# Kernel optimization log

Measured on AMD Instinct MI355X. Metric: run time of the kernel, lower is better.

## Reference

```python
import jax, jax.numpy as jnp
import numpy as np

MV = 16          # multivector dimension (PGA G(3,0,1))
BLADE_LEN = 9    # number of equivariant basis maps
# inner-product mask: coordinates not containing e0 (scalar, e1,e2,e3, e12,e13,e23, e123)
IP_IDX = np.array([0, 2, 3, 4, 8, 9, 10, 14])


def equi_linear(w, blade, x):
    """EquiLinearLayer: einsum('j i b, b x y, ... i x -> ... j y').
    Precompute blade-contracted weight once (fusion the kernel would do)."""
    wb = jnp.einsum('jib,bxy->jixy', w, blade)          # [J, I, MV, MV]
    return jnp.einsum('jixy,...ix->...jy', wb, x)        # [..., J, MV]


def setup_inputs() -> dict:
    key = jax.random.key(0)
    ks = jax.random.split(key, 6)
    B, N, C = 2, 2048, 64       # batch, items, mv_channels
    D, H = 64, 8                # hidden_dim, n_heads
    x = jax.random.normal(ks[0], (B, N, C, MV), dtype=jnp.float32)
    blade = jax.random.normal(ks[1], (BLADE_LEN, MV, MV), dtype=jnp.float32)
    w_q = jax.random.uniform(ks[2], (D * H, C, BLADE_LEN), dtype=jnp.float32)
    w_k = jax.random.uniform(ks[3], (D, C, BLADE_LEN), dtype=jnp.float32)
    w_v = jax.random.uniform(ks[4], (D, C, BLADE_LEN), dtype=jnp.float32)
    w_o = jax.random.uniform(ks[5], (C, D * H, BLADE_LEN), dtype=jnp.float32)
    return {"x": x, "blade": blade, "w_q": w_q, "w_k": w_k, "w_v": w_v, "w_o": w_o}


def reference(x, blade, w_q, w_k, w_v, w_o):
    B, N, C, _ = x.shape
    D = w_k.shape[0]
    H = w_q.shape[0] // D

    q = equi_linear(w_q, blade, x)   # [B, N, D*H, MV]
    k = equi_linear(w_k, blade, x)   # [B, N, D, MV]
    v = equi_linear(w_v, blade, x)   # [B, N, D, MV]

    # '(hidden_dim n_heads)' split: hidden_dim outer, heads inner
    q = q.reshape(B, N, D, H, MV).transpose(0, 3, 1, 2, 4)   # [B, H, N, D, MV]

    # select inner-product coordinates and flatten channel x coord
    qm = q[..., IP_IDX].reshape(B, H, N, D * len(IP_IDX))    # [B, H, N, D*8]
    km = k[..., IP_IDX].reshape(B, N, D * len(IP_IDX))        # [B, N, D*8]
    vf = v.reshape(B, N, D * MV)                              # [B, N, D*16]

    scale = 1.0 / jnp.sqrt(jnp.asarray(qm.shape[-1], qm.dtype))
    scores = jnp.einsum('bhqe,bke->bhqk', qm, km) * scale     # [B, H, N, N]
    attn = jax.nn.softmax(scores, axis=-1)
    out = jnp.einsum('bhqk,bkf->bhqf', attn, vf)              # [B, H, N, D*16]

    # slice first hidden_dim*mv (a no-op here since v keeps all 16 coords)
    out = out[..., : D * MV].reshape(B, H, N, D, MV)
    # '(heads hidden_dim)': heads outer
    out = out.transpose(0, 2, 1, 3, 4).reshape(B, N, H * D, MV)

    return equi_linear(w_o, blade, out)                       # [B, N, out_channels, MV]
```

## Files before the change

kernel.cpp:

```cpp
#include <hip/hip_runtime.h>
#include <math.h>


typedef __bf16 bf16x8 __attribute__((ext_vector_type(8)));
typedef __bf16 bf16x4 __attribute__((ext_vector_type(4)));
typedef float floatx4 __attribute__((ext_vector_type(4)));
typedef float floatx16 __attribute__((ext_vector_type(16)));

__constant__ int c_ip[8] = {0, 2, 3, 4, 8, 9, 10, 14};

__global__ __launch_bounds__(256) void prep2(
    const float* __restrict__ x, const float* __restrict__ blade,
    const float* __restrict__ w_q, const float* __restrict__ w_k,
    const float* __restrict__ w_v, const float* __restrict__ w_o,
    __bf16* __restrict__ xh, __bf16* __restrict__ xl,
    __bf16* __restrict__ wbqkh, __bf16* __restrict__ wbqkl,
    __bf16* __restrict__ wbv, __bf16* __restrict__ wbo)
{
  __shared__ float sw[4608];
  __shared__ float sbl[144];
  const int blk = blockIdx.x;
  const int tid = threadIdx.x;

  if (blk < 4608) {
    int n = blk;
    const float* wrow;
    int y;
    if (n < 4096) {
      int e = n & 7, d = (n >> 3) & 63, h = n >> 9;
      wrow = w_q + (size_t)(d * 8 + h) * 576;
      y = c_ip[e];
    } else {
      int n2 = n - 4096;
      int e = n2 & 7, d = n2 >> 3;
      wrow = w_k + (size_t)d * 576;
      y = c_ip[e];
    }
    for (int t = tid; t < 576; t += 256) sw[t] = wrow[t];
    if (tid < 144) sbl[tid] = blade[(tid >> 4) * 256 + (tid & 15) * 16 + y];
    __syncthreads();
#pragma unroll
    for (int kq = 0; kq < 4; kq++) {
      int k = kq * 256 + tid;
      int i = k >> 4, xx = k & 15;
      float s = 0.f;
#pragma unroll
      for (int b = 0; b < 9; b++) s += sw[i * 9 + b] * sbl[b * 16 + xx];
      __bf16 h16 = (__bf16)s;
      wbqkh[(size_t)n * 1024 + k] = h16;
      wbqkl[(size_t)n * 1024 + k] = (__bf16)(s - (float)h16);
    }
  } else if (blk < 5632) {
    int n = blk - 4608;
    int d = n >> 4, y = n & 15;
    const float* wrow = w_v + (size_t)d * 576;
    for (int t = tid; t < 576; t += 256) sw[t] = wrow[t];
    if (tid < 144) sbl[tid] = blade[(tid >> 4) * 256 + (tid & 15) * 16 + y];
    __syncthreads();
#pragma unroll
    for (int kq = 0; kq < 4; kq++) {
      int k = kq * 256 + tid;
      int i = k >> 4, xx = k & 15;
      float s = 0.f;
#pragma unroll
      for (int b = 0; b < 9; b++) s += sw[i * 9 + b] * sbl[b * 16 + xx];
      wbv[(size_t)n * 1024 + k] = (__bf16)s;
    }
  } else if (blk < 6656) {
    int n = blk - 5632;
    int c = n >> 4, y = n & 15;
    const float* wrow = w_o + (size_t)c * 4608;
    for (int t = tid; t < 4608; t += 256) sw[t] = wrow[t];
    if (tid < 144) sbl[tid] = blade[(tid >> 4) * 256 + (tid & 15) * 16 + y];
    __syncthreads();
#pragma unroll
    for (int kq = 0; kq < 32; kq++) {
      int k = kq * 256 + tid;
      int ich = (k >> 10) * 64 + ((k >> 4) & 63);
      int mv = k & 15;
      float s = 0.f;
#pragma unroll
      for (int b = 0; b < 9; b++) s += sw[ich * 9 + b] * sbl[b * 16 + mv];
      wbo[(size_t)n * 8192 + k] = (__bf16)s;
    }
  } else {
    int idx = (blk - 6656) * 256 + tid;
    float4 v = ((const float4*)x)[idx];
    bf16x4 h, l;
    h.x = (__bf16)v.x; l.x = (__bf16)(v.x - (float)h.x);
    h.y = (__bf16)v.y; l.y = (__bf16)(v.y - (float)h.y);
    h.z = (__bf16)v.z; l.z = (__bf16)(v.z - (float)h.z);
    h.w = (__bf16)v.w; l.w = (__bf16)(v.w - (float)h.w);
    *(bf16x4*)(xh + (size_t)idx * 4) = h;
    *(bf16x4*)(xl + (size_t)idx * 4) = l;
  }
}

__global__ __launch_bounds__(256) void reduce4(
    const float* __restrict__ p, float* __restrict__ out, int n)
{
  int i = (blockIdx.x * 256 + threadIdx.x) * 4;
  if (i >= n) return;
  float4 a = *(const float4*)(p + i);
  float4 b = *(const float4*)(p + (size_t)n + i);
  float4 c = *(const float4*)(p + 2 * (size_t)n + i);
  float4 d = *(const float4*)(p + 3 * (size_t)n + i);
  *(float4*)(out + i) = make_float4(a.x + b.x + c.x + d.x, a.y + b.y + c.y + d.y,
                                    a.z + b.z + c.z + d.z, a.w + b.w + c.w + d.w);
}

static __device__ __forceinline__ void gll16(const __bf16* g, __bf16* l) {
  __builtin_amdgcn_global_load_lds(
      (const __attribute__((address_space(1))) void*)g,
      (__attribute__((address_space(3))) void*)l, 16, 0, 0);
}

template <int GROUP, int TS>
static __device__ __forceinline__ void swizzle_mn(int& m0, int& n0) {
  int gn = gridDim.x;
  int flat = blockIdx.y * gn + blockIdx.x;
  int panel = flat / (GROUP * gn);
  int r = flat - panel * GROUP * gn;
  m0 = (panel * GROUP + (r % GROUP)) * TS;
  n0 = (r / GROUP) * TS;
}

template <int GROUP, int TSM, int TSN>
static __device__ __forceinline__ void swizzle_mn2(int& m0, int& n0) {
  int gn = gridDim.x;
  int flat = blockIdx.y * gn + blockIdx.x;
  int panel = flat / (GROUP * gn);
  int r = flat - panel * GROUP * gn;
  m0 = (panel * GROUP + (r % GROUP)) * TSM;
  n0 = (r / GROUP) * TSN;
}

static __device__ __forceinline__ int frag_off32(int row, int t, int kh) {
  return row * 32 + 8 * ((2 * t + kh) ^ ((row >> 1) & 3));
}

template <int EPI>
__global__ __launch_bounds__(256) void gemm_bf16(
    const __bf16* __restrict__ A, int lda, long long sAz,
    const __bf16* __restrict__ Bt, int ldb, long long sBz,
    void* __restrict__ C0v, int ldc, long long sCz,
    int K, float alpha)
{
  __shared__ __bf16 As[128 * 32];
  __shared__ __bf16 Bs[128 * 32];
  const int tid = threadIdx.x;
  const int wave = tid >> 6, lane = tid & 63;
  int m0, n0;
  swizzle_mn<4, 128>(m0, n0);
  A  += (size_t)blockIdx.z * sAz;
  Bt += (size_t)blockIdx.z * sBz;

  const int srow = lane >> 2;
  const int skk = 8 * ((lane & 3) ^ ((lane >> 3) & 3));
  const __bf16* gA0 = A  + (size_t)(m0 + wave * 32      + srow) * lda + skk;
  const __bf16* gA1 = A  + (size_t)(m0 + wave * 32 + 16 + srow) * lda + skk;
  const __bf16* gB0 = Bt + (size_t)(n0 + wave * 32      + srow) * ldb + skk;
  const __bf16* gB1 = Bt + (size_t)(n0 + wave * 32 + 16 + srow) * ldb + skk;
  const int ldsoff = wave * 1024;

  const int l31 = lane & 31, kh = lane >> 5;
  const int wm = (wave & 1) * 64, wn = (wave >> 1) * 64;
  int aoff[2][2], boff[2][2];
#pragma unroll
  for (int i = 0; i < 2; i++)
#pragma unroll
    for (int t = 0; t < 2; t++) {
      aoff[i][t] = frag_off32(wm + i * 32 + l31, t, kh);
      boff[i][t] = frag_off32(wn + i * 32 + l31, t, kh);
    }

  floatx16 acc[2][2];
#pragma unroll
  for (int i = 0; i < 2; i++)
#pragma unroll
    for (int j = 0; j < 2; j++)
#pragma unroll
      for (int e = 0; e < 16; e++) acc[i][j][e] = 0.f;

  for (int k0 = 0; k0 < K; k0 += 32) {
    gll16(gA0, As + ldsoff); gll16(gA1, As + ldsoff + 512);
    gll16(gB0, Bs + ldsoff); gll16(gB1, Bs + ldsoff + 512);
    gA0 += 32; gA1 += 32; gB0 += 32; gB1 += 32;
    __syncthreads();
    bf16x8 af[2][2], bfv[2][2];
#pragma unroll
    for (int i = 0; i < 2; i++)
#pragma unroll
      for (int t = 0; t < 2; t++) {
        af[i][t]  = *(const bf16x8*)(As + aoff[i][t]);
        bfv[i][t] = *(const bf16x8*)(Bs + boff[i][t]);
      }
#pragma unroll
    for (int t = 0; t < 2; t++)
#pragma unroll
      for (int i = 0; i < 2; i++)
#pragma unroll
        for (int j = 0; j < 2; j++)
          acc[i][j] = __builtin_amdgcn_mfma_f32_32x32x16_bf16(
              af[i][t], bfv[j][t], acc[i][j], 0, 0, 0);
    __syncthreads();
  }

  const int rb = m0 + wm + 4 * kh;
  const int cb = n0 + wn + l31;
#pragma unroll
  for (int i = 0; i < 2; i++) {
#pragma unroll
    for (int j = 0; j < 2; j++) {
      int c = cb + j * 32;
#pragma unroll
      for (int q = 0; q < 4; q++) {
        int r = rb + i * 32 + 8 * q;
        float v0 = acc[i][j][q * 4 + 0] * alpha;
        float v1 = acc[i][j][q * 4 + 1] * alpha;
        float v2 = acc[i][j][q * 4 + 2] * alpha;
        float v3 = acc[i][j][q * 4 + 3] * alpha;
        if (EPI == 0) {
          float* C = (float*)C0v + (size_t)blockIdx.z * sCz;
          float* p = C + (size_t)r * ldc + c;
          p[0] = v0; p[ldc] = v1; p[2 * ldc] = v2; p[3 * ldc] = v3;
        } else {
          __bf16* C = (__bf16*)C0v + (size_t)blockIdx.z * sCz;
          C[(size_t)r * ldc + c] = (__bf16)v0;
          C[(size_t)(r + 1) * ldc + c] = (__bf16)v1;
          C[(size_t)(r + 2) * ldc + c] = (__bf16)v2;
          C[(size_t)(r + 3) * ldc + c] = (__bf16)v3;
        }
      }
    }
  }
}

template <int EPI>
__global__ __launch_bounds__(256) void gemm_split(
    const __bf16* __restrict__ Ah, const __bf16* __restrict__ Al, int lda, long long sAz,
    const __bf16* __restrict__ Bh, const __bf16* __restrict__ Bl, int ldb, long long sBz,
    void* __restrict__ C0v, void* __restrict__ C1v, int ldc, long long sCz,
    int K, float alpha)
{
  __shared__ __bf16 Ash[128 * 32];
  __shared__ __bf16 Asl[128 * 32];
  __shared__ __bf16 Bsh[128 * 32];
  __shared__ __bf16 Bsl[128 * 32];
  const int tid = threadIdx.x;
  const int wave = tid >> 6, lane = tid & 63;
  int m0, n0;
  swizzle_mn<8, 128>(m0, n0);
  Ah += (size_t)blockIdx.z * sAz;
  Al += (size_t)blockIdx.z * sAz;
  Bh += (size_t)blockIdx.z * sBz;
  Bl += (size_t)blockIdx.z * sBz;

  const int srow = lane >> 2;
  const int skk = 8 * ((lane & 3) ^ ((lane >> 3) & 3));
  const size_t ao0 = (size_t)(m0 + wave * 32      + srow) * lda + skk;
  const size_t ao1 = (size_t)(m0 + wave * 32 + 16 + srow) * lda + skk;
  const size_t bo0 = (size_t)(n0 + wave * 32      + srow) * ldb + skk;
  const size_t bo1 = (size_t)(n0 + wave * 32 + 16 + srow) * ldb + skk;
  const __bf16 *gAh0 = Ah + ao0, *gAh1 = Ah + ao1;
  const __bf16 *gAl0 = Al + ao0, *gAl1 = Al + ao1;
  const __bf16 *gBh0 = Bh + bo0, *gBh1 = Bh + bo1;
  const __bf16 *gBl0 = Bl + bo0, *gBl1 = Bl + bo1;
  const int ldsoff = wave * 1024;

  const int fr = lane & 15, fq = lane >> 4;
  const int wm = (wave & 1) * 64, wn = (wave >> 1) * 64;
  int aoff[4], boff[4];
#pragma unroll
  for (int t = 0; t < 4; t++) {
    int rA = wm + t * 16 + fr;
    aoff[t] = rA * 32 + 8 * (fq ^ ((rA >> 1) & 3));
    int rB = wn + t * 16 + fr;
    boff[t] = rB * 32 + 8 * (fq ^ ((rB >> 1) & 3));
  }

  floatx4 acc[4][4];
#pragma unroll
  for (int i = 0; i < 4; i++)
#pragma unroll
    for (int j = 0; j < 4; j++) acc[i][j] = (floatx4){0.f, 0.f, 0.f, 0.f};

  for (int k0 = 0; k0 < K; k0 += 32) {
    gll16(gAh0, Ash + ldsoff); gll16(gAh1, Ash + ldsoff + 512);
    gll16(gAl0, Asl + ldsoff); gll16(gAl1, Asl + ldsoff + 512);
    gll16(gBh0, Bsh + ldsoff); gll16(gBh1, Bsh + ldsoff + 512);
    gll16(gBl0, Bsl + ldsoff); gll16(gBl1, Bsl + ldsoff + 512);
    gAh0 += 32; gAh1 += 32; gAl0 += 32; gAl1 += 32;
    gBh0 += 32; gBh1 += 32; gBl0 += 32; gBl1 += 32;
    __syncthreads();
    bf16x8 afh[4], afl[4], bfh[4], bfl[4];
#pragma unroll
    for (int t = 0; t < 4; t++) {
      afh[t] = *(const bf16x8*)(Ash + aoff[t]);
      afl[t] = *(const bf16x8*)(Asl + aoff[t]);
      bfh[t] = *(const bf16x8*)(Bsh + boff[t]);
      bfl[t] = *(const bf16x8*)(Bsl + boff[t]);
    }
#pragma unroll
    for (int i = 0; i < 4; i++)
#pragma unroll
      for (int j = 0; j < 4; j++) {
        acc[i][j] = __builtin_amdgcn_mfma_f32_16x16x32_bf16(
            afh[i], bfh[j], acc[i][j], 0, 0, 0);
        acc[i][j] = __builtin_amdgcn_mfma_f32_16x16x32_bf16(
            afl[i], bfh[j], acc[i][j], 0, 0, 0);
        acc[i][j] = __builtin_amdgcn_mfma_f32_16x16x32_bf16(
            afh[i], bfl[j], acc[i][j], 0, 0, 0);
      }
    __syncthreads();
  }

  const int rb = m0 + wm + fq * 4;
  const int cb = n0 + wn + fr;
#pragma unroll
  for (int i = 0; i < 4; i++) {
#pragma unroll
    for (int j = 0; j < 4; j++) {
      float vv[4] = {acc[i][j].x * alpha, acc[i][j].y * alpha,
                     acc[i][j].z * alpha, acc[i][j].w * alpha};
      int r = rb + i * 16, c = cb + j * 16;
      if (EPI == 0) {
        float* C = (float*)C0v + (size_t)blockIdx.z * sCz;
        float* p = C + (size_t)r * ldc + c;
        p[0] = vv[0]; p[ldc] = vv[1]; p[2 * ldc] = vv[2]; p[3 * ldc] = vv[3];
      } else {
        __bf16* Hp = (__bf16*)C0v + (size_t)blockIdx.z * sCz;
        __bf16* Lp = (__bf16*)C1v + (size_t)blockIdx.z * sCz;
#pragma unroll
        for (int t = 0; t < 4; t++) {
          size_t o = (size_t)(r + t) * ldc + c;
          __bf16 hh = (__bf16)vv[t];
          Hp[o] = hh;
          Lp[o] = (__bf16)(vv[t] - (float)hh);
        }
      }
    }
  }
}

#define MFMA1(a, b, c) c = __builtin_amdgcn_mfma_f32_16x16x32_bf16(a, b, c, 0, 0, 0)

#define MFMA_PAIR2(A0H, A0L, A1H, A1L, i0, i1)                              \
  __builtin_amdgcn_s_setprio(1);                                            \
  _Pragma("unroll") for (int j = 0; j < 4; j++) {                           \
    MFMA1(A0H, bh[j], acc[i0][j]); MFMA1(A1H, bh[j], acc[i1][j]);           \
    MFMA1(A0L, bh[j], acc[i0][j]); MFMA1(A1L, bh[j], acc[i1][j]);           \
    MFMA1(A0H, bl[j], acc[i0][j]); MFMA1(A1H, bl[j], acc[i1][j]);           \
  }                                                                         \
  __builtin_amdgcn_s_setprio(0)

#define TILE8P(SAh, SAl, SBh, SBl, DAh, DAl, DBh, DBl, PF)                  \
  do {                                                                      \
    bf16x8 bh[4], bl[4];                                                    \
    _Pragma("unroll") for (int j = 0; j < 4; j++) {                         \
      bh[j] = *(const bf16x8*)(SBh + boff[j]);                              \
      bl[j] = *(const bf16x8*)(SBl + boff[j]);                              \
    }                                                                       \
    bf16x8 a0h0 = *(const bf16x8*)(SAh + aoff[0]);                          \
    bf16x8 a0l0 = *(const bf16x8*)(SAl + aoff[0]);                          \
    bf16x8 a1h0 = *(const bf16x8*)(SAh + aoff[1]);                          \
    bf16x8 a1l0 = *(const bf16x8*)(SAl + aoff[1]);                          \
                  \
    bf16x8 a0h1 = *(const bf16x8*)(SAh + aoff[2]);                          \
    bf16x8 a0l1 = *(const bf16x8*)(SAl + aoff[2]);                          \
    bf16x8 a1h1 = *(const bf16x8*)(SAh + aoff[3]);                          \
    bf16x8 a1l1 = *(const bf16x8*)(SAl + aoff[3]);                          \
    if (PF) { gll16(pAh0, DAh + lw); gll16(pAh1, DAh + lw + 512);           \
              gll16(pAl0, DAl + lw);                                        \
              pAh0 += 32; pAh1 += 32; pAl0 += 32; }                         \
    MFMA_PAIR2(a0h0, a0l0, a1h0, a1l0, 0, 1);                               \
                  \
    bf16x8 a0h2 = *(const bf16x8*)(SAh + aoff[4]);                          \
    bf16x8 a0l2 = *(const bf16x8*)(SAl + aoff[4]);                          \
    bf16x8 a1h2 = *(const bf16x8*)(SAh + aoff[5]);                          \
    bf16x8 a1l2 = *(const bf16x8*)(SAl + aoff[5]);                          \
    if (PF) { gll16(pAl1, DAl + lw + 512);                                  \
              gll16(pBh0, DBh + lw); gll16(pBh1, DBh + lw + 512);           \
              pAl1 += 32; pBh0 += 32; pBh1 += 32; }                         \
    MFMA_PAIR2(a0h1, a0l1, a1h1, a1l1, 2, 3);                               \
                  \
    bf16x8 a0h3 = *(const bf16x8*)(SAh + aoff[6]);                          \
    bf16x8 a0l3 = *(const bf16x8*)(SAl + aoff[6]);                          \
    bf16x8 a1h3 = *(const bf16x8*)(SAh + aoff[7]);                          \
    bf16x8 a1l3 = *(const bf16x8*)(SAl + aoff[7]);                          \
    if (PF) { gll16(pBl0, DBl + lw); gll16(pBl1, DBl + lw + 512);           \
              pBl0 += 32; pBl1 += 32; }                                     \
    MFMA_PAIR2(a0h2, a0l2, a1h2, a1l2, 4, 5);                               \
                          \
    MFMA_PAIR2(a0h3, a0l3, a1h3, a1l3, 6, 7);                               \
    __syncthreads();                                                        \
  } while (0)

template <int EPI>
__global__ __launch_bounds__(512) void gemm_split_8p(
    const __bf16* __restrict__ Ah, const __bf16* __restrict__ Al, int lda, long long sAz,
    const __bf16* __restrict__ Bh, const __bf16* __restrict__ Bl, int ldb, long long sBz,
    void* __restrict__ C0v, void* __restrict__ C1v, int ldc, long long sCz,
    int K, float alpha)
{
  __shared__ __bf16 sAh0[256 * 32], sAl0[256 * 32], sBh0[256 * 32], sBl0[256 * 32];
  __shared__ __bf16 sAh1[256 * 32], sAl1[256 * 32], sBh1[256 * 32], sBl1[256 * 32];
  const int tid = threadIdx.x;
  const int wave = tid >> 6, lane = tid & 63;
  int m0, n0;
  swizzle_mn<4, 256>(m0, n0);
  Ah += (size_t)blockIdx.z * sAz;
  Al += (size_t)blockIdx.z * sAz;
  Bh += (size_t)blockIdx.z * sBz;
  Bl += (size_t)blockIdx.z * sBz;

  const int srow = lane >> 2;
  const int skk = 8 * ((lane & 3) ^ ((lane >> 3) & 3));
  const __bf16* pAh0 = Ah + (size_t)(m0 + wave * 32 + srow) * lda + skk;
  const __bf16* pAh1 = pAh0 + (size_t)16 * lda;
  const __bf16* pAl0 = Al + (size_t)(m0 + wave * 32 + srow) * lda + skk;
  const __bf16* pAl1 = pAl0 + (size_t)16 * lda;
  const __bf16* pBh0 = Bh + (size_t)(n0 + wave * 32 + srow) * ldb + skk;
  const __bf16* pBh1 = pBh0 + (size_t)16 * ldb;
  const __bf16* pBl0 = Bl + (size_t)(n0 + wave * 32 + srow) * ldb + skk;
  const __bf16* pBl1 = pBl0 + (size_t)16 * ldb;
  const int lw = wave * 1024;

  const int fr = lane & 15, fq = lane >> 4;
  const int wm = (wave >> 2) * 128, wn = (wave & 3) * 64;
  int aoff[8], boff[4];
#pragma unroll
  for (int i = 0; i < 8; i++) {
    int rA = wm + i * 16 + fr;
    aoff[i] = rA * 32 + 8 * (fq ^ ((rA >> 1) & 3));
  }
#pragma unroll
  for (int j = 0; j < 4; j++) {
    int rB = wn + j * 16 + fr;
    boff[j] = rB * 32 + 8 * (fq ^ ((rB >> 1) & 3));
  }

  floatx4 acc[8][4];
#pragma unroll
  for (int i = 0; i < 8; i++)
#pragma unroll
    for (int j = 0; j < 4; j++) acc[i][j] = (floatx4){0.f, 0.f, 0.f, 0.f};

  const int ktiles = K >> 5;

  gll16(pAh0, sAh0 + lw); gll16(pAh1, sAh0 + lw + 512); pAh0 += 32; pAh1 += 32;
  gll16(pAl0, sAl0 + lw); gll16(pAl1, sAl0 + lw + 512); pAl0 += 32; pAl1 += 32;
  gll16(pBh0, sBh0 + lw); gll16(pBh1, sBh0 + lw + 512); pBh0 += 32; pBh1 += 32;
  gll16(pBl0, sBl0 + lw); gll16(pBl1, sBl0 + lw + 512); pBl0 += 32; pBl1 += 32;
  __syncthreads();

  for (int it = 0; it < (ktiles >> 1); ++it) {
    TILE8P(sAh0, sAl0, sBh0, sBl0, sAh1, sAl1, sBh1, sBl1,
           (2 * it + 1 < ktiles));
    TILE8P(sAh1, sAl1, sBh1, sBl1, sAh0, sAl0, sBh0, sBl0,
           (2 * it + 2 < ktiles));
  }

  const int rb = m0 + wm + fq * 4;
  const int cb = n0 + wn + fr;
#pragma unroll
  for (int i = 0; i < 8; i++) {
#pragma unroll
    for (int j = 0; j < 4; j++) {
      int r = rb + i * 16, c = cb + j * 16;
      float vv[4] = {acc[i][j].x * alpha, acc[i][j].y * alpha,
                     acc[i][j].z * alpha, acc[i][j].w * alpha};
      if (EPI == 0) {
        float* C = (float*)C0v + (size_t)blockIdx.z * sCz;
        float* p = C + (size_t)r * ldc + c;
        p[0] = vv[0]; p[ldc] = vv[1]; p[2 * ldc] = vv[2]; p[3 * ldc] = vv[3];
      } else {
        __bf16* Hp = (__bf16*)C0v + (size_t)blockIdx.z * sCz;
        __bf16* Lp = (__bf16*)C1v + (size_t)blockIdx.z * sCz;
#pragma unroll
        for (int t = 0; t < 4; t++) {
          size_t o = (size_t)(r + t) * ldc + c;
          __bf16 hh = (__bf16)vv[t];
          Hp[o] = hh;
          Lp[o] = (__bf16)(vv[t] - (float)hh);
        }
      }
    }
  }
}

#define PTILE(SA0, SA1, SB0, SB1, DA0, DA1, DB0, DB1, PF)                   \
  do {                                                                      \
    bf16x8 b0[4], b1[4];                                                    \
    _Pragma("unroll") for (int j = 0; j < 4; j++)                           \
      b0[j] = *(const bf16x8*)(SB0 + boff[j]);                              \
    bf16x8 a00 = *(const bf16x8*)(SA0 + aoff[0]);                           \
    bf16x8 a10 = *(const bf16x8*)(SA0 + aoff[1]);                           \
       \
    _Pragma("unroll") for (int j = 0; j < 4; j++)                           \
      b1[j] = *(const bf16x8*)(SB1 + boff[j]);                              \
    bf16x8 a01 = *(const bf16x8*)(SA1 + aoff[0]);                           \
    bf16x8 a11 = *(const bf16x8*)(SA1 + aoff[1]);                           \
    if (PF) { gll16(pA0, DA0 + lw); gll16(pA1, DA0 + lw + 512); }           \
    __builtin_amdgcn_s_setprio(1);                                          \
    _Pragma("unroll") for (int j = 0; j < 4; j++) {                         \
      MFMA1(a00, b0[j], acc[0][j]); MFMA1(a10, b0[j], acc[1][j]);           \
    }                                                                       \
    __builtin_amdgcn_s_setprio(0);                                          \
            \
    bf16x8 a20 = *(const bf16x8*)(SA0 + aoff[2]);                           \
    bf16x8 a30 = *(const bf16x8*)(SA0 + aoff[3]);                           \
    if (PF) { gll16(pA0 + 32, DA1 + lw); gll16(pA1 + 32, DA1 + lw + 512);   \
              pA0 += 64; pA1 += 64; }                                       \
    __builtin_amdgcn_s_setprio(1);                                          \
    _Pragma("unroll") for (int j = 0; j < 4; j++) {                         \
      MFMA1(a01, b1[j], acc[0][j]); MFMA1(a11, b1[j], acc[1][j]);           \
    }                                                                       \
    __builtin_amdgcn_s_setprio(0);                                          \
            \
    bf16x8 a21 = *(const bf16x8*)(SA1 + aoff[2]);                           \
    bf16x8 a31 = *(const bf16x8*)(SA1 + aoff[3]);                           \
    if (PF) { gll16(pB0, DB0 + lwB); gll16(pB0 + 32, DB1 + lwB);            \
              pB0 += 64; }                                                  \
    __builtin_amdgcn_s_setprio(1);                                          \
    _Pragma("unroll") for (int j = 0; j < 4; j++) {                         \
      MFMA1(a20, b0[j], acc[2][j]); MFMA1(a30, b0[j], acc[3][j]);           \
    }                                                                       \
    __builtin_amdgcn_s_setprio(0);                                          \
                  \
    __builtin_amdgcn_s_setprio(1);                                          \
    _Pragma("unroll") for (int j = 0; j < 4; j++) {                         \
      MFMA1(a21, b1[j], acc[2][j]); MFMA1(a31, b1[j], acc[3][j]);           \
    }                                                                       \
    __builtin_amdgcn_s_setprio(0);                                          \
    __syncthreads();                                                        \
  } while (0)

template <int EPI>
__global__ __launch_bounds__(512) void gemm_bf16_8p(
    const __bf16* __restrict__ A, int lda, long long sAz,
    const __bf16* __restrict__ Bt, int ldb, long long sBz,
    void* __restrict__ C0v, int ldc, long long sCz,
    int K, float alpha)
{
  __shared__ __bf16 sA0_0[256 * 32], sA1_0[256 * 32];
  __shared__ __bf16 sB0_0[128 * 32], sB1_0[128 * 32];
  __shared__ __bf16 sA0_1[256 * 32], sA1_1[256 * 32];
  __shared__ __bf16 sB0_1[128 * 32], sB1_1[128 * 32];
  const int tid = threadIdx.x;
  const int wave = tid >> 6, lane = tid & 63;
  int m0, n0;
  swizzle_mn2<4, 256, 128>(m0, n0);
  A  += (size_t)blockIdx.z * sAz;
  Bt += (size_t)blockIdx.z * sBz;

  const int srow = lane >> 2;
  const int skk = 8 * ((lane & 3) ^ ((lane >> 3) & 3));
  const __bf16* pA0 = A + (size_t)(m0 + wave * 32 + srow) * lda + skk;
  const __bf16* pA1 = pA0 + (size_t)16 * lda;
  const __bf16* pB0 = Bt + (size_t)(n0 + wave * 16 + srow) * ldb + skk;
  const int lw = wave * 1024;
  const int lwB = wave * 512;

  const int fr = lane & 15, fq = lane >> 4;
  const int wm = (wave >> 1) * 64, wn = (wave & 1) * 64;
  int aoff[4], boff[4];
#pragma unroll
  for (int i = 0; i < 4; i++) {
    int rA = wm + i * 16 + fr;
    aoff[i] = rA * 32 + 8 * (fq ^ ((rA >> 1) & 3));
    int rB = wn + i * 16 + fr;
    boff[i] = rB * 32 + 8 * (fq ^ ((rB >> 1) & 3));
  }

  floatx4 acc[4][4];
#pragma unroll
  for (int i = 0; i < 4; i++)
#pragma unroll
    for (int j = 0; j < 4; j++) acc[i][j] = (floatx4){0.f, 0.f, 0.f, 0.f};

  const int ktiles = K >> 6;

  gll16(pA0, sA0_0 + lw); gll16(pA1, sA0_0 + lw + 512);
  gll16(pA0 + 32, sA1_0 + lw); gll16(pA1 + 32, sA1_0 + lw + 512);
  gll16(pB0, sB0_0 + lwB); gll16(pB0 + 32, sB1_0 + lwB);
  pA0 += 64; pA1 += 64; pB0 += 64;
  __syncthreads();

  for (int it = 0; it < (ktiles >> 1); ++it) {
    PTILE(sA0_0, sA1_0, sB0_0, sB1_0, sA0_1, sA1_1, sB0_1, sB1_1,
          (2 * it + 1 < ktiles));
    PTILE(sA0_1, sA1_1, sB0_1, sB1_1, sA0_0, sA1_0, sB0_0, sB1_0,
          (2 * it + 2 < ktiles));
  }

  const int rb = m0 + wm + fq * 4;
  const int cb = n0 + wn + fr;
#pragma unroll
  for (int i = 0; i < 4; i++) {
#pragma unroll
    for (int j = 0; j < 4; j++) {
      int r = rb + i * 16, c = cb + j * 16;
      float vv[4] = {acc[i][j].x * alpha, acc[i][j].y * alpha,
                     acc[i][j].z * alpha, acc[i][j].w * alpha};
      if (EPI == 0) {
        float* C = (float*)C0v + (size_t)blockIdx.z * sCz;
        float* p = C + (size_t)r * ldc + c;
        p[0] = vv[0]; p[ldc] = vv[1]; p[2 * ldc] = vv[2]; p[3 * ldc] = vv[3];
      } else {
        __bf16* C = (__bf16*)C0v + (size_t)blockIdx.z * sCz;
        C[(size_t)r * ldc + c] = (__bf16)vv[0];
        C[(size_t)(r + 1) * ldc + c] = (__bf16)vv[1];
        C[(size_t)(r + 2) * ldc + c] = (__bf16)vv[2];
        C[(size_t)(r + 3) * ldc + c] = (__bf16)vv[3];
      }
    }
  }
}

__global__ __launch_bounds__(256) void softmax_wave(float* __restrict__ Pf)
{
  const int wave = threadIdx.x >> 6, lane = threadIdx.x & 63;
  const size_t row = (size_t)blockIdx.x * 4 + wave;
  float* p = Pf + row * 2048;
  __bf16* q = (__bf16*)p;

  float4 v[8];
  float m = -1e30f;
#pragma unroll
  for (int t = 0; t < 8; t++) {
    v[t] = ((const float4*)p)[lane + t * 64];
    m = fmaxf(m, fmaxf(fmaxf(v[t].x, v[t].y), fmaxf(v[t].z, v[t].w)));
  }
#pragma unroll
  for (int off = 32; off; off >>= 1) m = fmaxf(m, __shfl_xor(m, off, 64));

  float s = 0.f;
#pragma unroll
  for (int t = 0; t < 8; t++) {
    v[t].x = expf(v[t].x - m); v[t].y = expf(v[t].y - m);
    v[t].z = expf(v[t].z - m); v[t].w = expf(v[t].w - m);
    s += (v[t].x + v[t].y) + (v[t].z + v[t].w);
  }
#pragma unroll
  for (int off = 32; off; off >>= 1) s += __shfl_xor(s, off, 64);
  float inv = 1.0f / s;

#pragma unroll
  for (int t = 0; t < 8; t++) {
    bf16x4 o;
    o.x = (__bf16)(v[t].x * inv); o.y = (__bf16)(v[t].y * inv);
    o.z = (__bf16)(v[t].z * inv); o.w = (__bf16)(v[t].w * inv);
    *(bf16x4*)(q + (lane + t * 64) * 4) = o;
  }
}

extern "C" void kernel_launch(void* const* d_in, const int* in_sizes, int n_in,
                              void* d_out, int out_size, void* d_ws, size_t ws_size,
                              hipStream_t stream)
{
  (void)in_sizes; (void)n_in; (void)out_size; (void)ws_size;
  const float* x     = (const float*)d_in[0];
  const float* blade = (const float*)d_in[1];
  const float* w_q   = (const float*)d_in[2];
  const float* w_k   = (const float*)d_in[3];
  const float* w_v   = (const float*)d_in[4];
  const float* w_o   = (const float*)d_in[5];
  float* out = (float*)d_out;

  char* base = (char*)d_ws;
  __bf16* wbo   = (__bf16*)(base);
  __bf16* vT    = (__bf16*)(base + 16777216);
  __bf16* qkmh  = (__bf16*)(base + 25165824);
  __bf16* qkml  = (__bf16*)(base + 62914560);
  char* scr = base + 100663296;
  __bf16* xh    = (__bf16*)(scr);
  __bf16* xl    = (__bf16*)(scr + 8388608);
  __bf16* wbqkh = (__bf16*)(scr + 16777216);
  __bf16* wbqkl = (__bf16*)(scr + 26214400);
  __bf16* wbv   = (__bf16*)(scr + 35651584);
  float*  Pf    = (float*)(scr);
  __bf16* A2    = (__bf16*)(scr + 67108864);
  float*  Part  = (float*)(scr + 100663296);

  dim3 blk(256);
  const float scale = 0.04419417382415922f;

  prep2<<<10752, blk, 0, stream>>>(x, blade, w_q, w_k, w_v, w_o,
                                   xh, xl, wbqkh, wbqkl, wbv, wbo);

  gemm_split_8p<2><<<dim3(16, 16, 1), dim3(512), 0, stream>>>(
      xh, xl, 1024, 0, wbqkh, wbqkl, 1024, 0,
      qkmh, qkml, 4608, 0, 1024, 1.f);

  gemm_split<2><<<dim3(4, 32, 1), blk, 0, stream>>>(
      xh, xl, 1024, 0,
      wbqkh + (size_t)4096 * 1024, wbqkl + (size_t)4096 * 1024, 1024, 0,
      qkmh + 4096, qkml + 4096, 4608, 0, 1024, 1.f);

  gemm_bf16<3><<<dim3(32, 8, 1), blk, 0, stream>>>(
      wbv, 1024, 0, xh, 1024, 0, vT, 4096, 0, 1024, 1.f);

  for (int b = 0; b < 2; b++) {
    const __bf16* qh_b  = qkmh + (size_t)b * 2048 * 4608;
    const __bf16* ql_b  = qkml + (size_t)b * 2048 * 4608;
    const __bf16* kmh_b = qh_b + 4096;
    const __bf16* kml_b = ql_b + 4096;

    for (int h0 = 0; h0 < 8; h0 += 4) {
      gemm_split_8p<0><<<dim3(8, 8, 4), dim3(512), 0, stream>>>(
          qh_b + h0 * 512, ql_b + h0 * 512, 4608, 512,
          kmh_b, kml_b, 4608, 0,
          Pf, nullptr, 2048, (long long)2048 * 2048, 512, scale);
      softmax_wave<<<4 * 2048 / 4, blk, 0, stream>>>(Pf);
      gemm_bf16_8p<3><<<dim3(8, 8, 4), dim3(512), 0, stream>>>(
          (const __bf16*)Pf, 4096, (long long)2048 * 4096,
          vT + (size_t)b * 2048, 4096, 0,
          A2 + (size_t)h0 * 1024, 8192, 1024, 2048, 1.f);
    }

    gemm_bf16_8p<0><<<dim3(8, 8, 4), dim3(512), 0, stream>>>(
        A2, 8192, 2048, wbo, 8192, 2048,
        Part, 1024, (long long)2048 * 1024, 2048, 1.f);
    reduce4<<<2048, blk, 0, stream>>>(Part, out + (size_t)b * 2048 * 1024,
                                      2048 * 1024);
  }
}
```

Baseline: 737.0 us.

## Switch split-bf16 GEMM to 32x32x16 MFMA tiles and reorder PTILE fragment loads

```diff
diff --git a/kernel.cpp b/kernel.cpp
--- a/kernel.cpp
+++ b/kernel.cpp
@@ -343,56 +343,64 @@
   }
 }
 
-#define MFMA1(a, b, c) c = __builtin_amdgcn_mfma_f32_16x16x32_bf16(a, b, c, 0, 0, 0)
-
-#define MFMA_PAIR2(A0H, A0L, A1H, A1L, i0, i1)                              \
+#define MFMA32(a, b, c) c = __builtin_amdgcn_mfma_f32_32x32x16_bf16(a, b, c, 0, 0, 0)
+
+#define MFMA_FRAG32(I)                                                      \
   __builtin_amdgcn_s_setprio(1);                                            \
-  _Pragma("unroll") for (int j = 0; j < 4; j++) {                           \
-    MFMA1(A0H, bh[j], acc[i0][j]); MFMA1(A1H, bh[j], acc[i1][j]);           \
-    MFMA1(A0L, bh[j], acc[i0][j]); MFMA1(A1L, bh[j], acc[i1][j]);           \
-    MFMA1(A0H, bl[j], acc[i0][j]); MFMA1(A1H, bl[j], acc[i1][j]);           \
-  }                                                                         \
+  MFMA32(ah0, bh00, acc[I][0]); MFMA32(ah0, bh10, acc[I][1]);               \
+  MFMA32(al0, bh00, acc[I][0]); MFMA32(al0, bh10, acc[I][1]);               \
+  MFMA32(ah0, bl00, acc[I][0]); MFMA32(ah0, bl10, acc[I][1]);               \
+  MFMA32(ah1, bh01, acc[I][0]); MFMA32(ah1, bh11, acc[I][1]);               \
+  MFMA32(al1, bh01, acc[I][0]); MFMA32(al1, bh11, acc[I][1]);               \
+  MFMA32(ah1, bl01, acc[I][0]); MFMA32(ah1, bl11, acc[I][1]);               \
   __builtin_amdgcn_s_setprio(0)
 
 #define TILE8P(SAh, SAl, SBh, SBl, DAh, DAl, DBh, DBl, PF)                  \
   do {                                                                      \
-    bf16x8 bh[4], bl[4];                                                    \
-    _Pragma("unroll") for (int j = 0; j < 4; j++) {                         \
-      bh[j] = *(const bf16x8*)(SBh + boff[j]);                              \
-      bl[j] = *(const bf16x8*)(SBl + boff[j]);                              \
+    bf16x8 bh00 = *(const bf16x8*)(SBh + boff[0][0]);                       \
+    bf16x8 bh01 = *(const bf16x8*)(SBh + boff[0][1]);                       \
+    bf16x8 bh10 = *(const bf16x8*)(SBh + boff[1][0]);                       \
+    bf16x8 bh11 = *(const bf16x8*)(SBh + boff[1][1]);                       \
+    bf16x8 bl00 = *(const bf16x8*)(SBl + boff[0][0]);                       \
+    bf16x8 bl01 = *(const bf16x8*)(SBl + boff[0][1]);                       \
+    bf16x8 bl10 = *(const bf16x8*)(SBl + boff[1][0]);                       \
+    bf16x8 bl11 = *(const bf16x8*)(SBl + boff[1][1]);                       \
+    {                              \
+      bf16x8 ah0 = *(const bf16x8*)(SAh + aoff[0][0]);                      \
+      bf16x8 ah1 = *(const bf16x8*)(SAh + aoff[0][1]);                      \
+      bf16x8 al0 = *(const bf16x8*)(SAl + aoff[0][0]);                      \
+      bf16x8 al1 = *(const bf16x8*)(SAl + aoff[0][1]);                      \
+      if (PF) { gll16(pAh0, DAh + lw); gll16(pAh1, DAh + lw + 512);         \
+                gll16(pAl0, DAl + lw);                                      \
+                pAh0 += 32; pAh1 += 32; pAl0 += 32; }                       \
+      MFMA_FRAG32(0);                                                       \
     }                                                                       \
-    bf16x8 a0h0 = *(const bf16x8*)(SAh + aoff[0]);                          \
-    bf16x8 a0l0 = *(const bf16x8*)(SAl + aoff[0]);                          \
-    bf16x8 a1h0 = *(const bf16x8*)(SAh + aoff[1]);                          \
-    bf16x8 a1l0 = *(const bf16x8*)(SAl + aoff[1]);                          \
-                  \
-    bf16x8 a0h1 = *(const bf16x8*)(SAh + aoff[2]);                          \
-    bf16x8 a0l1 = *(const bf16x8*)(SAl + aoff[2]);                          \
-    bf16x8 a1h1 = *(const bf16x8*)(SAh + aoff[3]);                          \
-    bf16x8 a1l1 = *(const bf16x8*)(SAl + aoff[3]);                          \
-    if (PF) { gll16(pAh0, DAh + lw); gll16(pAh1, DAh + lw + 512);           \
-              gll16(pAl0, DAl + lw);                                        \
-              pAh0 += 32; pAh1 += 32; pAl0 += 32; }                         \
-    MFMA_PAIR2(a0h0, a0l0, a1h0, a1l0, 0, 1);                               \
-                  \
-    bf16x8 a0h2 = *(const bf16x8*)(SAh + aoff[4]);                          \
-    bf16x8 a0l2 = *(const bf16x8*)(SAl + aoff[4]);                          \
-    bf16x8 a1h2 = *(const bf16x8*)(SAh + aoff[5]);                          \
-    bf16x8 a1l2 = *(const bf16x8*)(SAl + aoff[5]);                          \
-    if (PF) { gll16(pAl1, DAl + lw + 512);                                  \
-              gll16(pBh0, DBh + lw); gll16(pBh1, DBh + lw + 512);           \
-              pAl1 += 32; pBh0 += 32; pBh1 += 32; }                         \
-    MFMA_PAIR2(a0h1, a0l1, a1h1, a1l1, 2, 3);                               \
-                  \
-    bf16x8 a0h3 = *(const bf16x8*)(SAh + aoff[6]);                          \
-    bf16x8 a0l3 = *(const bf16x8*)(SAl + aoff[6]);                          \
-    bf16x8 a1h3 = *(const bf16x8*)(SAh + aoff[7]);                          \
-    bf16x8 a1l3 = *(const bf16x8*)(SAl + aoff[7]);                          \
-    if (PF) { gll16(pBl0, DBl + lw); gll16(pBl1, DBl + lw + 512);           \
-              pBl0 += 32; pBl1 += 32; }                                     \
-    MFMA_PAIR2(a0h2, a0l2, a1h2, a1l2, 4, 5);                               \
-                          \
-    MFMA_PAIR2(a0h3, a0l3, a1h3, a1l3, 6, 7);                               \
+    {                              \
+      bf16x8 ah0 = *(const bf16x8*)(SAh + aoff[1][0]);                      \
+      bf16x8 ah1 = *(const bf16x8*)(SAh + aoff[1][1]);                      \
+      bf16x8 al0 = *(const bf16x8*)(SAl + aoff[1][0]);                      \
+      bf16x8 al1 = *(const bf16x8*)(SAl + aoff[1][1]);                      \
+      if (PF) { gll16(pAl1, DAl + lw + 512);                                \
+                gll16(pBh0, DBh + lw); gll16(pBh1, DBh + lw + 512);         \
+                pAl1 += 32; pBh0 += 32; pBh1 += 32; }                       \
+      MFMA_FRAG32(1);                                                       \
+    }                                                                       \
+    {                              \
+      bf16x8 ah0 = *(const bf16x8*)(SAh + aoff[2][0]);                      \
+      bf16x8 ah1 = *(const bf16x8*)(SAh + aoff[2][1]);                      \
+      bf16x8 al0 = *(const bf16x8*)(SAl + aoff[2][0]);                      \
+      bf16x8 al1 = *(const bf16x8*)(SAl + aoff[2][1]);                      \
+      if (PF) { gll16(pBl0, DBl + lw); gll16(pBl1, DBl + lw + 512);         \
+                pBl0 += 32; pBl1 += 32; }                                   \
+      MFMA_FRAG32(2);                                                       \
+    }                                                                       \
+    {          \
+      bf16x8 ah0 = *(const bf16x8*)(SAh + aoff[3][0]);                      \
+      bf16x8 ah1 = *(const bf16x8*)(SAh + aoff[3][1]);                      \
+      bf16x8 al0 = *(const bf16x8*)(SAl + aoff[3][0]);                      \
+      bf16x8 al1 = *(const bf16x8*)(SAl + aoff[3][1]);                      \
+      MFMA_FRAG32(3);                                                       \
+    }                                                                       \
     __syncthreads();                                                        \
   } while (0)
 
@@ -426,25 +434,27 @@
   const __bf16* pBl1 = pBl0 + (size_t)16 * ldb;
   const int lw = wave * 1024;
 
-  const int fr = lane & 15, fq = lane >> 4;
+  const int l31 = lane & 31, kh = lane >> 5;
   const int wm = (wave >> 2) * 128, wn = (wave & 3) * 64;
-  int aoff[8], boff[4];
-#pragma unroll
-  for (int i = 0; i < 8; i++) {
-    int rA = wm + i * 16 + fr;
-    aoff[i] = rA * 32 + 8 * (fq ^ ((rA >> 1) & 3));
-  }
-#pragma unroll
-  for (int j = 0; j < 4; j++) {
-    int rB = wn + j * 16 + fr;
-    boff[j] = rB * 32 + 8 * (fq ^ ((rB >> 1) & 3));
-  }
-
-  floatx4 acc[8][4];
-#pragma unroll
-  for (int i = 0; i < 8; i++)
-#pragma unroll
-    for (int j = 0; j < 4; j++) acc[i][j] = (floatx4){0.f, 0.f, 0.f, 0.f};
+  int aoff[4][2], boff[2][2];
+#pragma unroll
+  for (int i = 0; i < 4; i++)
+#pragma unroll
+    for (int t = 0; t < 2; t++)
+      aoff[i][t] = frag_off32(wm + i * 32 + l31, t, kh);
+#pragma unroll
+  for (int j = 0; j < 2; j++)
+#pragma unroll
+    for (int t = 0; t < 2; t++)
+      boff[j][t] = frag_off32(wn + j * 32 + l31, t, kh);
+
+  floatx16 acc[4][2];
+#pragma unroll
+  for (int i = 0; i < 4; i++)
+#pragma unroll
+    for (int j = 0; j < 2; j++)
+#pragma unroll
+      for (int e = 0; e < 16; e++) acc[i][j][e] = 0.f;
 
   const int ktiles = K >> 5;
 
@@ -461,55 +471,62 @@
            (2 * it + 2 < ktiles));
   }
 
-  const int rb = m0 + wm + fq * 4;
-  const int cb = n0 + wn + fr;
-#pragma unroll
-  for (int i = 0; i < 8; i++) {
-#pragma unroll
-    for (int j = 0; j < 4; j++) {
-      int r = rb + i * 16, c = cb + j * 16;
-      float vv[4] = {acc[i][j].x * alpha, acc[i][j].y * alpha,
-                     acc[i][j].z * alpha, acc[i][j].w * alpha};
-      if (EPI == 0) {
-        float* C = (float*)C0v + (size_t)blockIdx.z * sCz;
-        float* p = C + (size_t)r * ldc + c;
-        p[0] = vv[0]; p[ldc] = vv[1]; p[2 * ldc] = vv[2]; p[3 * ldc] = vv[3];
-      } else {
-        __bf16* Hp = (__bf16*)C0v + (size_t)blockIdx.z * sCz;
-        __bf16* Lp = (__bf16*)C1v + (size_t)blockIdx.z * sCz;
-#pragma unroll
-        for (int t = 0; t < 4; t++) {
-          size_t o = (size_t)(r + t) * ldc + c;
-          __bf16 hh = (__bf16)vv[t];
-          Hp[o] = hh;
-          Lp[o] = (__bf16)(vv[t] - (float)hh);
+  const int rb = m0 + wm + 4 * kh;
+  const int cb = n0 + wn + l31;
+#pragma unroll
+  for (int i = 0; i < 4; i++) {
+#pragma unroll
+    for (int j = 0; j < 2; j++) {
+      int c = cb + j * 32;
+#pragma unroll
+      for (int q = 0; q < 4; q++) {
+        int r = rb + i * 32 + 8 * q;
+        float v0 = acc[i][j][q * 4 + 0] * alpha;
+        float v1 = acc[i][j][q * 4 + 1] * alpha;
+        float v2 = acc[i][j][q * 4 + 2] * alpha;
+        float v3 = acc[i][j][q * 4 + 3] * alpha;
+        if (EPI == 0) {
+          float* C = (float*)C0v + (size_t)blockIdx.z * sCz;
+          float* p = C + (size_t)r * ldc + c;
+          p[0] = v0; p[ldc] = v1; p[2 * ldc] = v2; p[3 * ldc] = v3;
+        } else {
+          __bf16* Hp = (__bf16*)C0v + (size_t)blockIdx.z * sCz;
+          __bf16* Lp = (__bf16*)C1v + (size_t)blockIdx.z * sCz;
+          float vv[4] = {v0, v1, v2, v3};
+#pragma unroll
+          for (int s = 0; s < 4; s++) {
+            size_t o = (size_t)(r + s) * ldc + c;
+            __bf16 hh = (__bf16)vv[s];
+            Hp[o] = hh;
+            Lp[o] = (__bf16)(vv[s] - (float)hh);
+          }
         }
       }
     }
   }
 }
 
+#define MFMA1(a, b, c) c = __builtin_amdgcn_mfma_f32_16x16x32_bf16(a, b, c, 0, 0, 0)
+
 #define PTILE(SA0, SA1, SB0, SB1, DA0, DA1, DB0, DB1, PF)                   \
   do {                                                                      \
+                \
     bf16x8 b0[4], b1[4];                                                    \
     _Pragma("unroll") for (int j = 0; j < 4; j++)                           \
       b0[j] = *(const bf16x8*)(SB0 + boff[j]);                              \
     bf16x8 a00 = *(const bf16x8*)(SA0 + aoff[0]);                           \
     bf16x8 a10 = *(const bf16x8*)(SA0 + aoff[1]);                           \
-       \
-    _Pragma("unroll") for (int j = 0; j < 4; j++)                           \
-      b1[j] = *(const bf16x8*)(SB1 + boff[j]);                              \
-    bf16x8 a01 = *(const bf16x8*)(SA1 + aoff[0]);                           \
-    bf16x8 a11 = *(const bf16x8*)(SA1 + aoff[1]);                           \
     if (PF) { gll16(pA0, DA0 + lw); gll16(pA1, DA0 + lw + 512); }           \
     __builtin_amdgcn_s_setprio(1);                                          \
     _Pragma("unroll") for (int j = 0; j < 4; j++) {                         \
       MFMA1(a00, b0[j], acc[0][j]); MFMA1(a10, b0[j], acc[1][j]);           \
     }                                                                       \
     __builtin_amdgcn_s_setprio(0);                                          \
-            \
-    bf16x8 a20 = *(const bf16x8*)(SA0 + aoff[2]);                           \
-    bf16x8 a30 = *(const bf16x8*)(SA0 + aoff[3]);                           \
+                \
+    _Pragma("unroll") for (int j = 0; j < 4; j++)                           \
+      b1[j] = *(const bf16x8*)(SB1 + boff[j]);                              \
+    bf16x8 a01 = *(const bf16x8*)(SA1 + aoff[0]);                           \
+    bf16x8 a11 = *(const bf16x8*)(SA1 + aoff[1]);                           \
     if (PF) { gll16(pA0 + 32, DA1 + lw); gll16(pA1 + 32, DA1 + lw + 512);   \
               pA0 += 64; pA1 += 64; }                                       \
     __builtin_amdgcn_s_setprio(1);                                          \
@@ -517,9 +534,9 @@
       MFMA1(a01, b1[j], acc[0][j]); MFMA1(a11, b1[j], acc[1][j]);           \
     }                                                                       \
     __builtin_amdgcn_s_setprio(0);                                          \
-            \
-    bf16x8 a21 = *(const bf16x8*)(SA1 + aoff[2]);                           \
-    bf16x8 a31 = *(const bf16x8*)(SA1 + aoff[3]);                           \
+                           \
+    bf16x8 a20 = *(const bf16x8*)(SA0 + aoff[2]);                           \
+    bf16x8 a30 = *(const bf16x8*)(SA0 + aoff[3]);                           \
     if (PF) { gll16(pB0, DB0 + lwB); gll16(pB0 + 32, DB1 + lwB);            \
               pB0 += 64; }                                                  \
     __builtin_amdgcn_s_setprio(1);                                          \
@@ -527,7 +544,9 @@
       MFMA1(a20, b0[j], acc[2][j]); MFMA1(a30, b0[j], acc[3][j]);           \
     }                                                                       \
     __builtin_amdgcn_s_setprio(0);                                          \
-                  \
+           \
+    bf16x8 a21 = *(const bf16x8*)(SA1 + aoff[2]);                           \
+    bf16x8 a31 = *(const bf16x8*)(SA1 + aoff[3]);                           \
     __builtin_amdgcn_s_setprio(1);                                          \
     _Pragma("unroll") for (int j = 0; j < 4; j++) {                         \
       MFMA1(a21, b1[j], acc[2][j]); MFMA1(a31, b1[j], acc[3][j]);           \
```

Result: slower. 755.2 us (+2.5%).
